# Kernel tuning notes

Hardware: AMD Instinct MI355X
Metric: run time of the kernel (lower is better)

Reference implementation:

```python
import jax, jax.numpy as jnp
import numpy as np

N = 100000
IN_DIM = 256
OUT_DIM = 256
E = 3200000
SLOPE = 0.2


def setup_inputs() -> dict:
    key = jax.random.key(0)
    ks = jax.random.split(key, 14)
    xav = lambda k, shape: jax.random.normal(k, shape, jnp.float32) * np.sqrt(2.0 / sum(shape))
    inp = {
        "H": jax.random.normal(ks[0], (N, IN_DIM), jnp.float32),
        "W0": xav(ks[1], (IN_DIM, OUT_DIM)),
        "W1": xav(ks[2], (IN_DIM, OUT_DIM)),
        "W2": xav(ks[3], (IN_DIM, OUT_DIM)),
        "a0": xav(ks[4], (2 * OUT_DIM,)),
        "a1": xav(ks[5], (2 * OUT_DIM,)),
        "a2": xav(ks[6], (2 * OUT_DIM,)),
        "bias": jnp.zeros((OUT_DIM,), jnp.float32),
    }
    for i, r in enumerate(["0", "1", "2"]):
        inp["row" + r] = jax.random.randint(ks[7 + 2 * i], (E,), 0, N, jnp.int32)
        inp["col" + r] = jax.random.randint(ks[8 + 2 * i], (E,), 0, N, jnp.int32)
    return inp


def _gat_type(H, W, a, row, col):
    # Wh: [N, out_dim]
    Wh = H @ W
    # attention logits per edge: leaky_relu(a_dst . Wh[row] + a_src . Wh[col])
    s_dst = Wh @ a[:OUT_DIM]   # [N]
    s_src = Wh @ a[OUT_DIM:]   # [N]
    e = jax.nn.leaky_relu(s_dst[row] + s_src[col], SLOPE)  # [E]
    # segment softmax over destination node (row)
    e_max = jax.ops.segment_max(e, row, num_segments=N)    # [N]
    e_shifted = jnp.exp(e - e_max[row])
    e_sum = jax.ops.segment_sum(e_shifted, row, num_segments=N)
    alpha = e_shifted / jnp.maximum(e_sum[row], 1e-12)     # [E]
    # weighted aggregation of source features into destinations
    return jax.ops.segment_sum(alpha[:, None] * Wh[col], row, num_segments=N)


def reference(H, row0, col0, row1, col1, row2, col2, W0, W1, W2, a0, a1, a2, bias):
    out = _gat_type(H, W0, a0, row0, col0)
    out = out + _gat_type(H, W1, a1, row1, col1)
    out = out + _gat_type(H, W2, a2, row2, col2)
    return out + bias
```

## Files before the change

kernel.cpp:

```cpp
#include <hip/hip_runtime.h>
#include <cstdint>
#include <cstddef>

#define DIM 256
#define SLOPE 0.2f
#define BSHIFT 8
#define SLOTS 9216
#define TILE 4096

typedef __attribute__((ext_vector_type(8))) short short8;
typedef __attribute__((ext_vector_type(4))) float f32x4;

__device__ __forceinline__ unsigned short f2bf(float f) {
  unsigned u = __float_as_uint(f);
  u += 0x7fffu + ((u >> 16) & 1u);
  return (unsigned short)(u >> 16);
}
__device__ __forceinline__ float bf2f(unsigned short h) {
  return __uint_as_float(((unsigned)h) << 16);
}

__global__ void wtrans_kernel(const float* __restrict__ W0, const float* __restrict__ W1,
                              const float* __restrict__ W2, unsigned short* __restrict__ Wt) {
  const float* W = blockIdx.y == 0 ? W0 : (blockIdx.y == 1 ? W1 : W2);
  int k = blockIdx.x, n = threadIdx.x;
  Wt[((size_t)blockIdx.y * DIM + n) * DIM + k] = f2bf(W[k * DIM + n]);
}

__global__ __launch_bounds__(256, 2) void gemm3_scores_kernel(
    const float* __restrict__ H, const unsigned short* __restrict__ Wt,
    const float* __restrict__ a0, const float* __restrict__ a1,
    const float* __restrict__ a2, unsigned short* __restrict__ Whb,
    float* __restrict__ s_dst, float* __restrict__ s_src, int N, size_t wstride) {
  __shared__ unsigned short Hs[128][264];
  __shared__ unsigned short Os[4][4][264];
  const int t = threadIdx.x;
  const int r0 = blockIdx.x * 128;
#pragma unroll
  for (int i = 0; i < 32; ++i) {
    int idx = t + i * 256;
    int row = idx >> 6;
    int c4 = idx & 63;
    int r = r0 + row;
    float4 h = (r < N) ? *(const float4*)&H[(size_t)r * DIM + c4 * 4]
                       : make_float4(0.f, 0.f, 0.f, 0.f);
    unsigned lo = (unsigned)f2bf(h.x) | ((unsigned)f2bf(h.y) << 16);
    unsigned hi = (unsigned)f2bf(h.z) | ((unsigned)f2bf(h.w) << 16);
    *(uint2*)&Hs[row][c4 * 4] = make_uint2(lo, hi);
  }
  __syncthreads();
  const int wave = t >> 6, lane = t & 63;
  const int q = lane >> 4, m = lane & 15;
  const int rowbase = wave * 32;
  short8 Af0[8], Af1[8];
#pragma unroll
  for (int k0 = 0; k0 < 8; ++k0) {
    Af0[k0] = *(const short8*)&Hs[rowbase + m][k0 * 32 + q * 8];
    Af1[k0] = *(const short8*)&Hs[rowbase + 16 + m][k0 * 32 + q * 8];
  }
  const float* aptr[3] = {a0, a1, a2};
  for (int ty = 0; ty < 3; ++ty) {
    const unsigned short* Wtt = Wt + (size_t)ty * DIM * DIM;
    const float* a = aptr[ty];
    f32x4 acc0[16], acc1[16];
#pragma unroll
    for (int j = 0; j < 16; ++j) {
      acc0[j] = (f32x4){0.f, 0.f, 0.f, 0.f};
      acc1[j] = (f32x4){0.f, 0.f, 0.f, 0.f};
    }
#pragma unroll
    for (int k0 = 0; k0 < 8; ++k0) {
#pragma unroll
      for (int j = 0; j < 16; ++j) {
        short8 Bf = *(const short8*)&Wtt[(size_t)(j * 16 + m) * DIM + k0 * 32 + q * 8];
        acc0[j] = __builtin_amdgcn_mfma_f32_16x16x32_bf16(Af0[k0], Bf, acc0[j], 0, 0, 0);
        acc1[j] = __builtin_amdgcn_mfma_f32_16x16x32_bf16(Af1[k0], Bf, acc1[j], 0, 0, 0);
      }
    }
    float pd0[4] = {0, 0, 0, 0}, ps0[4] = {0, 0, 0, 0};
    float pd1[4] = {0, 0, 0, 0}, ps1[4] = {0, 0, 0, 0};
#pragma unroll
    for (int j = 0; j < 16; ++j) {
      int col = j * 16 + m;
      float ad = a[col], as = a[DIM + col];
#pragma unroll
      for (int reg = 0; reg < 4; ++reg) {
        float v0 = acc0[j][reg], v1 = acc1[j][reg];
        pd0[reg] += v0 * ad;
        ps0[reg] += v0 * as;
        pd1[reg] += v1 * ad;
        ps1[reg] += v1 * as;
      }
    }
#pragma unroll
    for (int off = 8; off >= 1; off >>= 1) {
#pragma unroll
      for (int reg = 0; reg < 4; ++reg) {
        pd0[reg] += __shfl_down(pd0[reg], off);
        ps0[reg] += __shfl_down(ps0[reg], off);
        pd1[reg] += __shfl_down(pd1[reg], off);
        ps1[reg] += __shfl_down(ps1[reg], off);
      }
    }
    if (m == 0) {
#pragma unroll
      for (int reg = 0; reg < 4; ++reg) {
        int ra = r0 + rowbase + q * 4 + reg;
        int rb = ra + 16;
        if (ra < N) {
          s_dst[(size_t)ty * N + ra] = pd0[reg];
          s_src[(size_t)ty * N + ra] = ps0[reg];
        }
        if (rb < N) {
          s_dst[(size_t)ty * N + rb] = pd1[reg];
          s_src[(size_t)ty * N + rb] = ps1[reg];
        }
      }
    }
    unsigned short* wout = Whb + (size_t)ty * wstride;
#pragma unroll
    for (int g = 0; g < 2; ++g) {
#pragma unroll
      for (int p = 0; p < 4; ++p) {
        if (q == p) {
#pragma unroll
          for (int j = 0; j < 16; ++j)
#pragma unroll
            for (int reg = 0; reg < 4; ++reg)
              Os[wave][reg][j * 16 + m] = f2bf(g ? acc1[j][reg] : acc0[j][reg]);
        }
#pragma unroll
        for (int rr = 0; rr < 4; ++rr) {
          int r = r0 + rowbase + g * 16 + p * 4 + rr;
          if (r < N)
            *(uint2*)&wout[(size_t)r * DIM + lane * 4] =
                *(const uint2*)&Os[wave][rr][lane * 4];
        }
      }
    }
  }
}

__global__ __launch_bounds__(256, 2) void gemm_scores_kernel(
    const float* __restrict__ H, const unsigned short* __restrict__ Wt,
    const float* __restrict__ a, unsigned short* __restrict__ Whb,
    float* __restrict__ s_dst, float* __restrict__ s_src, int N) {
  __shared__ unsigned short Hs[64][264];
  __shared__ unsigned short Os[4][16][264];
  const int t = threadIdx.x;
  const int r0 = blockIdx.x * 64;
#pragma unroll
  for (int i = 0; i < 16; ++i) {
    int idx = t + i * 256;
    int row = idx >> 6;
    int c4 = idx & 63;
    int r = r0 + row;
    float4 h = (r < N) ? *(const float4*)&H[(size_t)r * DIM + c4 * 4]
                       : make_float4(0.f, 0.f, 0.f, 0.f);
    unsigned lo = (unsigned)f2bf(h.x) | ((unsigned)f2bf(h.y) << 16);
    unsigned hi = (unsigned)f2bf(h.z) | ((unsigned)f2bf(h.w) << 16);
    *(uint2*)&Hs[row][c4 * 4] = make_uint2(lo, hi);
  }
  __syncthreads();
  const int wave = t >> 6, lane = t & 63;
  const int q = lane >> 4, m = lane & 15;
  const int rowbase = wave * 16;
  short8 Af[8];
#pragma unroll
  for (int k0 = 0; k0 < 8; ++k0)
    Af[k0] = *(const short8*)&Hs[rowbase + m][k0 * 32 + q * 8];
  f32x4 acc[16];
#pragma unroll
  for (int j = 0; j < 16; ++j) acc[j] = (f32x4){0.f, 0.f, 0.f, 0.f};
#pragma unroll
  for (int k0 = 0; k0 < 8; ++k0) {
#pragma unroll
    for (int j = 0; j < 16; ++j) {
      short8 Bf = *(const short8*)&Wt[(size_t)(j * 16 + m) * DIM + k0 * 32 + q * 8];
      acc[j] = __builtin_amdgcn_mfma_f32_16x16x32_bf16(Af[k0], Bf, acc[j], 0, 0, 0);
    }
  }
  float pd[4] = {0, 0, 0, 0}, ps[4] = {0, 0, 0, 0};
#pragma unroll
  for (int j = 0; j < 16; ++j) {
    int col = j * 16 + m;
    float ad = a[col], as = a[DIM + col];
#pragma unroll
    for (int reg = 0; reg < 4; ++reg) {
      float v = acc[j][reg];
      pd[reg] += v * ad;
      ps[reg] += v * as;
      Os[wave][q * 4 + reg][col] = f2bf(v);
    }
  }
#pragma unroll
  for (int off = 8; off >= 1; off >>= 1) {
#pragma unroll
    for (int reg = 0; reg < 4; ++reg) {
      pd[reg] += __shfl_down(pd[reg], off);
      ps[reg] += __shfl_down(ps[reg], off);
    }
  }
  if (m == 0) {
#pragma unroll
    for (int reg = 0; reg < 4; ++reg) {
      int r = r0 + rowbase + q * 4 + reg;
      if (r < N) {
        s_dst[r] = pd[reg];
        s_src[r] = ps[reg];
      }
    }
  }
  __syncthreads();
#pragma unroll
  for (int row = 0; row < 16; ++row) {
    int r = r0 + rowbase + row;
    if (r < N)
      *(uint2*)&Whb[(size_t)r * DIM + lane * 4] = *(const uint2*)&Os[wave][row][lane * 4];
  }
}

__global__ __launch_bounds__(256) void bin_edges_kernel(
    const int* __restrict__ r0, const int* __restrict__ r1, const int* __restrict__ r2,
    const int* __restrict__ c0, const int* __restrict__ c1, const int* __restrict__ c2,
    int* __restrict__ bcnt,
    unsigned* __restrict__ pairs,
    int E, int NB) {
  __shared__ int hist[512];
  __shared__ int curs[512];
  const int ty = blockIdx.y;
  const int* rr = ty == 0 ? r0 : (ty == 1 ? r1 : r2);
  const int* cc = ty == 0 ? c0 : (ty == 1 ? c1 : c2);
  const int t = threadIdx.x;
  const int base = blockIdx.x * TILE;
  for (int i = t; i < NB; i += 256) hist[i] = 0;
  __syncthreads();
  int rows[TILE / 256];
#pragma unroll
  for (int i = 0; i < TILE / 256; ++i) {
    int e = base + t + i * 256;
    int r = (e < E) ? rr[e] : -1;
    rows[i] = r;
    if (r >= 0) atomicAdd(&hist[r >> BSHIFT], 1);
  }
  __syncthreads();
  for (int b = t; b < NB; b += 256) {
    int h = hist[b];
    int off = h ? atomicAdd(&bcnt[ty * NB + b], h) : 0;
    curs[b] = b * SLOTS + off;
  }
  __syncthreads();
  unsigned* pt = pairs + (size_t)ty * NB * SLOTS;
#pragma unroll
  for (int i = 0; i < TILE / 256; ++i) {
    int e = base + t + i * 256;
    if (e >= E) continue;
    int r = rows[i];
    int b = r >> BSHIFT;
    int pos = atomicAdd(&curs[b], 1);
    if (pos - b * SLOTS < SLOTS)
      pt[pos] = ((unsigned)(r & 255) << 17) | (unsigned)cc[e];
  }
}

__global__ __launch_bounds__(256) void bucket_sort_kernel(
    const int* __restrict__ bcnt, unsigned* __restrict__ pairs,
    int* __restrict__ rp, int* __restrict__ deg, int N, int NB) {
  __shared__ int hist[256];
  __shared__ int excl[256];
  __shared__ int curs[256];
  __shared__ unsigned stage[SLOTS];
  const int b = blockIdx.x, ty = blockIdx.y;
  const int t = threadIdx.x;
  int cnt = bcnt[ty * NB + b];
  if (cnt > SLOTS) cnt = SLOTS;
  unsigned* pb = pairs + (size_t)ty * NB * SLOTS + (size_t)b * SLOTS;
  hist[t] = 0;
  __syncthreads();
  for (int i = t; i < cnt; i += 256) atomicAdd(&hist[pb[i] >> 17], 1);
  __syncthreads();
  int v = hist[t];
  excl[t] = v;
  __syncthreads();
  for (int off = 1; off < 256; off <<= 1) {
    int u = (t >= off) ? excl[t - off] : 0;
    __syncthreads();
    excl[t] += u;
    __syncthreads();
  }
  int ex = excl[t] - v;
  curs[t] = ex;
  int r = (b << BSHIFT) + t;
  if (r < N) {
    rp[(size_t)ty * N + r] = b * SLOTS + ex;
    deg[(size_t)ty * N + r] = v;
  }
  __syncthreads();
  for (int i = t; i < cnt; i += 256) {
    unsigned p = pb[i];
    int pos = atomicAdd(&curs[p >> 17], 1);
    stage[pos] = p;
  }
  __syncthreads();
  for (int i = t; i < cnt; i += 256) pb[i] = stage[i];
}

__global__ __launch_bounds__(256) void gat_fused_kernel(
    const int* __restrict__ rp, const int* __restrict__ deg,
    const unsigned* __restrict__ pairs,
    const float* __restrict__ s_dst, const float* __restrict__ s_src,
    const unsigned short* __restrict__ Whb,
    const float* __restrict__ bias, float* __restrict__ out, int N, int NB,
    size_t wstride) {
  __shared__ uint2 ebuf[4][64];
  int n = (int)((blockIdx.x * (unsigned)blockDim.x + threadIdx.x) >> 6);
  if (n >= N) return;
  const int wid = (threadIdx.x >> 6);
  const int lane = threadIdx.x & 63;
  float4 total = {0.f, 0.f, 0.f, 0.f};
  for (int t = 0; t < 3; ++t) {
    int beg = rp[(size_t)t * N + n], d = deg[(size_t)t * N + n];
    if (d == 0) continue;
    int end = beg + d;
    const unsigned* pcol = pairs + (size_t)t * NB * SLOTS;
    const float* ss = s_src + (size_t)t * N;
    float sd = s_dst[(size_t)t * N + n];
    const unsigned short* wbase = Whb + (size_t)t * wstride + lane * 4;
    float mx = -__builtin_inff();
    for (int p = beg + lane; p < end; p += 64) {
      float v = sd + ss[pcol[p] & 0x1FFFFu];
      v = v > 0.f ? v : SLOPE * v;
      mx = fmaxf(mx, v);
    }
#pragma unroll
    for (int off = 32; off >= 1; off >>= 1) mx = fmaxf(mx, __shfl_down(mx, off));
    mx = __shfl(mx, 0);
    float4 acc = {0.f, 0.f, 0.f, 0.f};
    float psum = 0.f;
    for (int base = beg; base < end; base += 64) {
      int myp = base + lane;
      int cnt = end - base;
      if (cnt > 64) cnt = 64;
      unsigned myc = 0;
      float mype = 0.f;
      if (myp < end) {
        myc = pcol[myp] & 0x1FFFFu;
        float v = sd + ss[myc];
        v = v > 0.f ? v : SLOPE * v;
        mype = __expf(v - mx);
      }
      psum += mype;
      ebuf[wid][lane] = make_uint2(myc, __float_as_uint(mype));
#pragma unroll 8
      for (int j = 0; j < cnt; ++j) {
        uint2 cp = ebuf[wid][j];
        float pe = __uint_as_float(cp.y);
        ushort4 w = *(const ushort4*)&wbase[(size_t)cp.x * DIM];
        acc.x += pe * bf2f(w.x);
        acc.y += pe * bf2f(w.y);
        acc.z += pe * bf2f(w.z);
        acc.w += pe * bf2f(w.w);
      }
    }
#pragma unroll
    for (int off = 32; off >= 1; off >>= 1) psum += __shfl_down(psum, off);
    psum = __shfl(psum, 0);
    float inv = 1.f / fmaxf(psum, 1e-12f);
    total.x += acc.x * inv;
    total.y += acc.y * inv;
    total.z += acc.z * inv;
    total.w += acc.w * inv;
  }
  float4 cur = ((const float4*)bias)[lane];
  cur.x += total.x;
  cur.y += total.y;
  cur.z += total.z;
  cur.w += total.w;
  *((float4*)(out + (size_t)n * DIM) + lane) = cur;
}

__global__ __launch_bounds__(256) void gat_node_kernel(
    const int* __restrict__ rp, const int* __restrict__ deg,
    const unsigned* __restrict__ pcol,
    const float* __restrict__ s_dst, const float* __restrict__ s_src,
    const unsigned short* __restrict__ Whb,
    const float* __restrict__ bias, float* __restrict__ out, int N, int first) {
  __shared__ uint2 ebuf[4][64];
  int n = (int)((blockIdx.x * (unsigned)blockDim.x + threadIdx.x) >> 6);
  if (n >= N) return;
  const int wid = (threadIdx.x >> 6);
  const int lane = threadIdx.x & 63;
  int beg = rp[n], d = deg[n], end = beg + d;
  if (!first && d == 0) return;
  float sd = s_dst[n];
  float mx = -__builtin_inff();
  for (int p = beg + lane; p < end; p += 64) {
    float v = sd + s_src[pcol[p] & 0x1FFFFu];
    v = v > 0.f ? v : SLOPE * v;
    mx = fmaxf(mx, v);
  }
#pragma unroll
  for (int off = 32; off >= 1; off >>= 1) mx = fmaxf(mx, __shfl_down(mx, off));
  mx = __shfl(mx, 0);
  const unsigned short* wbase = Whb + lane * 4;
  float4 acc = {0.f, 0.f, 0.f, 0.f};
  float psum = 0.f;
  for (int base = beg; base < end; base += 64) {
    int myp = base + lane;
    int cnt = end - base;
    if (cnt > 64) cnt = 64;
    unsigned myc = 0;
    float mype = 0.f;
    if (myp < end) {
      myc = pcol[myp] & 0x1FFFFu;
      float v = sd + s_src[myc];
      v = v > 0.f ? v : SLOPE * v;
      mype = __expf(v - mx);
    }
    psum += mype;
    ebuf[wid][lane] = make_uint2(myc, __float_as_uint(mype));
#pragma unroll 8
    for (int j = 0; j < cnt; ++j) {
      uint2 cp = ebuf[wid][j];
      float pe = __uint_as_float(cp.y);
      ushort4 w = *(const ushort4*)&wbase[(size_t)cp.x * DIM];
      acc.x += pe * bf2f(w.x);
      acc.y += pe * bf2f(w.y);
      acc.z += pe * bf2f(w.z);
      acc.w += pe * bf2f(w.w);
    }
  }
#pragma unroll
  for (int off = 32; off >= 1; off >>= 1) psum += __shfl_down(psum, off);
  psum = __shfl(psum, 0);
  float inv = 1.f / fmaxf(psum, 1e-12f);
  float4* o = (float4*)(out + (size_t)n * DIM) + lane;
  float4 cur = first ? ((const float4*)bias)[lane] : *o;
  cur.x += acc.x * inv;
  cur.y += acc.y * inv;
  cur.z += acc.z * inv;
  cur.w += acc.w * inv;
  *o = cur;
}

static inline size_t align256(size_t x) { return (x + 255) & ~(size_t)255; }

extern "C" void kernel_launch(void* const* d_in, const int* in_sizes, int n_in,
                              void* d_out, int out_size, void* d_ws, size_t ws_size,
                              hipStream_t stream) {
  const float* H = (const float*)d_in[0];
  const float* W[3] = {(const float*)d_in[1], (const float*)d_in[2], (const float*)d_in[3]};
  const float* a[3] = {(const float*)d_in[4], (const float*)d_in[5], (const float*)d_in[6]};
  const float* bias = (const float*)d_in[7];
  const int* row[3] = {(const int*)d_in[8], (const int*)d_in[10], (const int*)d_in[12]};
  const int* col[3] = {(const int*)d_in[9], (const int*)d_in[11], (const int*)d_in[13]};
  const int N = in_sizes[0] / DIM;
  const int E = in_sizes[8];
  const int NB = (N + 255) >> BSHIFT;
  float* out = (float*)d_out;

  char* ws = (char*)d_ws;
  size_t off = 0;
  unsigned short* Wt = (unsigned short*)(ws + off);
  off = align256(off + (size_t)3 * DIM * DIM * sizeof(unsigned short));
  float* s_dst = (float*)(ws + off);
  off = align256(off + (size_t)3 * N * sizeof(float));
  float* s_src = (float*)(ws + off);
  off = align256(off + (size_t)3 * N * sizeof(float));
  int* bcnt = (int*)(ws + off);
  off = align256(off + (size_t)3 * NB * sizeof(int));
  int* rp = (int*)(ws + off);
  off = align256(off + (size_t)3 * N * sizeof(int));
  int* deg = (int*)(ws + off);
  off = align256(off + (size_t)3 * N * sizeof(int));
  unsigned* pairs = (unsigned*)(ws + off);
  off = align256(off + (size_t)3 * NB * SLOTS * sizeof(unsigned));
  unsigned short* Whb = (unsigned short*)(ws + off);
  const size_t whb_bytes = align256((size_t)N * DIM * sizeof(unsigned short));
  const size_t wstride = whb_bytes / sizeof(unsigned short);
  const int fused = (ws_size >= off + 3 * whb_bytes) ? 1 : 0;

  wtrans_kernel<<<dim3(DIM, 3), 256, 0, stream>>>(W[0], W[1], W[2], Wt);
  hipMemsetAsync(bcnt, 0, (size_t)3 * NB * sizeof(int), stream);
  const int eb = (E + TILE - 1) / TILE;
  bin_edges_kernel<<<dim3(eb, 3), 256, 0, stream>>>(row[0], row[1], row[2], col[0], col[1],
                                                    col[2], bcnt, pairs, E, NB);
  bucket_sort_kernel<<<dim3(NB, 3), 256, 0, stream>>>(bcnt, pairs, rp, deg, N, NB);

  const int gat_blocks = (N * 64 + 255) / 256;
  if (fused) {
    gemm3_scores_kernel<<<(N + 127) / 128, 256, 0, stream>>>(H, Wt, a[0], a[1], a[2], Whb,
                                                             s_dst, s_src, N, wstride);
    gat_fused_kernel<<<gat_blocks, 256, 0, stream>>>(rp, deg, pairs, s_dst, s_src, Whb, bias,
                                                     out, N, NB, wstride);
  } else {
    for (int t = 0; t < 3; ++t) {
      gemm_scores_kernel<<<(N + 63) / 64, 256, 0, stream>>>(H, Wt + (size_t)t * DIM * DIM,
                                                            a[t], Whb, s_dst + (size_t)t * N,
                                                            s_src + (size_t)t * N, N);
      gat_node_kernel<<<gat_blocks, 256, 0, stream>>>(
          rp + (size_t)t * N, deg + (size_t)t * N, pairs + (size_t)t * NB * SLOTS,
          s_dst + (size_t)t * N, s_src + (size_t)t * N, Whb, bias, out, N, t == 0 ? 1 : 0);
    }
  }
  (void)n_in;
  (void)out_size;
  (void)ws_size;
}
```

Measured before the change: 1.426 ms.

## Merge independent prep and compute stages into combined horizontal-fused kernels

Weight transpose and edge binning now run as one prep kernel, with the block index choosing the role. The GEMM with scores and the per-bucket sort likewise share one compute kernel. Independent work can then overlap on the GPU and there are fewer launches and idle tails. The cost is that the combined kernel sizes its shared memory for the larger GEMM role, about 76 KB. Sort blocks therefore get the GEMM's occupancy limits, and the mixed kernel may use more registers.

```diff
diff --git a/kernel.cpp b/kernel.cpp
--- a/kernel.cpp
+++ b/kernel.cpp
@@ -20,22 +20,94 @@
   return __uint_as_float(((unsigned)h) << 16);
 }
 
-__global__ void wtrans_kernel(const float* __restrict__ W0, const float* __restrict__ W1,
-                              const float* __restrict__ W2, unsigned short* __restrict__ Wt) {
-  const float* W = blockIdx.y == 0 ? W0 : (blockIdx.y == 1 ? W1 : W2);
-  int k = blockIdx.x, n = threadIdx.x;
-  Wt[((size_t)blockIdx.y * DIM + n) * DIM + k] = f2bf(W[k * DIM + n]);
-}
-
-__global__ __launch_bounds__(256, 2) void gemm3_scores_kernel(
-    const float* __restrict__ H, const unsigned short* __restrict__ Wt,
+
+__device__ __forceinline__ void bin_edges_body(
+    int bx, int ty, int* hist, int* curs, const int* __restrict__ rr,
+    const int* __restrict__ cc, int* __restrict__ bcnt, unsigned* __restrict__ pairs,
+    int E, int NB) {
+  const int t = threadIdx.x;
+  const int base = bx * TILE;
+  for (int i = t; i < NB; i += 256) hist[i] = 0;
+  __syncthreads();
+  int rows[TILE / 256];
+#pragma unroll
+  for (int i = 0; i < TILE / 256; ++i) {
+    int e = base + t + i * 256;
+    int r = (e < E) ? rr[e] : -1;
+    rows[i] = r;
+    if (r >= 0) atomicAdd(&hist[r >> BSHIFT], 1);
+  }
+  __syncthreads();
+  for (int b = t; b < NB; b += 256) {
+    int h = hist[b];
+    int off = h ? atomicAdd(&bcnt[ty * NB + b], h) : 0;
+    curs[b] = b * SLOTS + off;
+  }
+  __syncthreads();
+  unsigned* pt = pairs + (size_t)ty * NB * SLOTS;
+#pragma unroll
+  for (int i = 0; i < TILE / 256; ++i) {
+    int e = base + t + i * 256;
+    if (e >= E) continue;
+    int r = rows[i];
+    int b = r >> BSHIFT;
+    int pos = atomicAdd(&curs[b], 1);
+    if (pos - b * SLOTS < SLOTS)
+      pt[pos] = ((unsigned)(r & 255) << 17) | (unsigned)cc[e];
+  }
+}
+
+__device__ __forceinline__ void bsort_body(
+    int b, int ty, char* smem, const int* __restrict__ bcnt,
+    unsigned* __restrict__ pairs, int* __restrict__ rp, int* __restrict__ deg,
+    int N, int NB) {
+  int* hist = (int*)smem;
+  int* excl = hist + 256;
+  int* curs = excl + 256;
+  unsigned* stage = (unsigned*)(curs + 256);
+  const int t = threadIdx.x;
+  int cnt = bcnt[ty * NB + b];
+  if (cnt > SLOTS) cnt = SLOTS;
+  unsigned* pb = pairs + (size_t)ty * NB * SLOTS + (size_t)b * SLOTS;
+  hist[t] = 0;
+  __syncthreads();
+  for (int i = t; i < cnt; i += 256) atomicAdd(&hist[pb[i] >> 17], 1);
+  __syncthreads();
+  int v = hist[t];
+  excl[t] = v;
+  __syncthreads();
+  for (int off = 1; off < 256; off <<= 1) {
+    int u = (t >= off) ? excl[t - off] : 0;
+    __syncthreads();
+    excl[t] += u;
+    __syncthreads();
+  }
+  int ex = excl[t] - v;
+  curs[t] = ex;
+  int r = (b << BSHIFT) + t;
+  if (r < N) {
+    rp[(size_t)ty * N + r] = b * SLOTS + ex;
+    deg[(size_t)ty * N + r] = v;
+  }
+  __syncthreads();
+  for (int i = t; i < cnt; i += 256) {
+    unsigned p = pb[i];
+    int pos = atomicAdd(&curs[p >> 17], 1);
+    stage[pos] = p;
+  }
+  __syncthreads();
+  for (int i = t; i < cnt; i += 256) pb[i] = stage[i];
+}
+
+__device__ __forceinline__ void gemm3_body(
+    int bx, char* smem, const float* __restrict__ H, const unsigned short* __restrict__ Wt,
     const float* __restrict__ a0, const float* __restrict__ a1,
     const float* __restrict__ a2, unsigned short* __restrict__ Whb,
     float* __restrict__ s_dst, float* __restrict__ s_src, int N, size_t wstride) {
-  __shared__ unsigned short Hs[128][264];
-  __shared__ unsigned short Os[4][4][264];
+  unsigned short(*Hs)[264] = (unsigned short(*)[264])smem;
+  unsigned short(*Os)[4][264] = (unsigned short(*)[4][264])(smem + 128 * 264 * 2);
   const int t = threadIdx.x;
-  const int r0 = blockIdx.x * 128;
+  const int r0 = bx * 128;
 #pragma unroll
   for (int i = 0; i < 32; ++i) {
     int idx = t + i * 256;
@@ -141,6 +213,52 @@
   }
 }
 
+
+__global__ __launch_bounds__(256) void prep_kernel(
+    const float* __restrict__ W0, const float* __restrict__ W1,
+    const float* __restrict__ W2, unsigned short* __restrict__ Wt,
+    const int* __restrict__ r0, const int* __restrict__ r1, const int* __restrict__ r2,
+    const int* __restrict__ c0, const int* __restrict__ c1, const int* __restrict__ c2,
+    int* __restrict__ bcnt, unsigned* __restrict__ pairs, int E, int NB, int eb) {
+  __shared__ int smem[1024];
+  const int bx = blockIdx.x;
+  if (bx < 768) {
+    int ty = bx >> 8, k = bx & 255, n = threadIdx.x;
+    const float* W = ty == 0 ? W0 : (ty == 1 ? W1 : W2);
+    Wt[((size_t)ty * DIM + n) * DIM + k] = f2bf(W[k * DIM + n]);
+    return;
+  }
+  int e2 = bx - 768;
+  int ty = e2 / eb, bxx = e2 % eb;
+  const int* rr = ty == 0 ? r0 : (ty == 1 ? r1 : r2);
+  const int* cc = ty == 0 ? c0 : (ty == 1 ? c1 : c2);
+  bin_edges_body(bxx, ty, smem, smem + 512, rr, cc, bcnt, pairs, E, NB);
+}
+
+__global__ __launch_bounds__(256, 2) void compute_kernel(
+    const float* __restrict__ H, const unsigned short* __restrict__ Wt,
+    const float* __restrict__ a0, const float* __restrict__ a1,
+    const float* __restrict__ a2, unsigned short* __restrict__ Whb,
+    float* __restrict__ s_dst, float* __restrict__ s_src, int N, size_t wstride,
+    const int* __restrict__ bcnt, unsigned* __restrict__ pairs,
+    int* __restrict__ rp, int* __restrict__ deg, int NB, int gemm_blocks) {
+  __shared__ __align__(16) char smem[76032];
+  const int bx = blockIdx.x;
+  if (bx < gemm_blocks) {
+    gemm3_body(bx, smem, H, Wt, a0, a1, a2, Whb, s_dst, s_src, N, wstride);
+  } else {
+    int e = bx - gemm_blocks;
+    bsort_body(e % NB, e / NB, smem, bcnt, pairs, rp, deg, N, NB);
+  }
+}
+
+__global__ __launch_bounds__(256) void bucket_sort_kernel(
+    const int* __restrict__ bcnt, unsigned* __restrict__ pairs,
+    int* __restrict__ rp, int* __restrict__ deg, int N, int NB) {
+  __shared__ __align__(16) char smem[39936];
+  bsort_body(blockIdx.x, blockIdx.y, smem, bcnt, pairs, rp, deg, N, NB);
+}
+
 __global__ __launch_bounds__(256, 2) void gemm_scores_kernel(
     const float* __restrict__ H, const unsigned short* __restrict__ Wt,
     const float* __restrict__ a, unsigned short* __restrict__ Whb,
@@ -218,91 +336,6 @@
     if (r < N)
       *(uint2*)&Whb[(size_t)r * DIM + lane * 4] = *(const uint2*)&Os[wave][row][lane * 4];
   }
-}
-
-__global__ __launch_bounds__(256) void bin_edges_kernel(
-    const int* __restrict__ r0, const int* __restrict__ r1, const int* __restrict__ r2,
-    const int* __restrict__ c0, const int* __restrict__ c1, const int* __restrict__ c2,
-    int* __restrict__ bcnt,
-    unsigned* __restrict__ pairs,
-    int E, int NB) {
-  __shared__ int hist[512];
-  __shared__ int curs[512];
-  const int ty = blockIdx.y;
-  const int* rr = ty == 0 ? r0 : (ty == 1 ? r1 : r2);
-  const int* cc = ty == 0 ? c0 : (ty == 1 ? c1 : c2);
-  const int t = threadIdx.x;
-  const int base = blockIdx.x * TILE;
-  for (int i = t; i < NB; i += 256) hist[i] = 0;
-  __syncthreads();
-  int rows[TILE / 256];
-#pragma unroll
-  for (int i = 0; i < TILE / 256; ++i) {
-    int e = base + t + i * 256;
-    int r = (e < E) ? rr[e] : -1;
-    rows[i] = r;
-    if (r >= 0) atomicAdd(&hist[r >> BSHIFT], 1);
-  }
-  __syncthreads();
-  for (int b = t; b < NB; b += 256) {
-    int h = hist[b];
-    int off = h ? atomicAdd(&bcnt[ty * NB + b], h) : 0;
-    curs[b] = b * SLOTS + off;
-  }
-  __syncthreads();
-  unsigned* pt = pairs + (size_t)ty * NB * SLOTS;
-#pragma unroll
-  for (int i = 0; i < TILE / 256; ++i) {
-    int e = base + t + i * 256;
-    if (e >= E) continue;
-    int r = rows[i];
-    int b = r >> BSHIFT;
-    int pos = atomicAdd(&curs[b], 1);
-    if (pos - b * SLOTS < SLOTS)
-      pt[pos] = ((unsigned)(r & 255) << 17) | (unsigned)cc[e];
-  }
-}
-
-__global__ __launch_bounds__(256) void bucket_sort_kernel(
-    const int* __restrict__ bcnt, unsigned* __restrict__ pairs,
-    int* __restrict__ rp, int* __restrict__ deg, int N, int NB) {
-  __shared__ int hist[256];
-  __shared__ int excl[256];
-  __shared__ int curs[256];
-  __shared__ unsigned stage[SLOTS];
-  const int b = blockIdx.x, ty = blockIdx.y;
-  const int t = threadIdx.x;
-  int cnt = bcnt[ty * NB + b];
-  if (cnt > SLOTS) cnt = SLOTS;
-  unsigned* pb = pairs + (size_t)ty * NB * SLOTS + (size_t)b * SLOTS;
-  hist[t] = 0;
-  __syncthreads();
-  for (int i = t; i < cnt; i += 256) atomicAdd(&hist[pb[i] >> 17], 1);
-  __syncthreads();
-  int v = hist[t];
-  excl[t] = v;
-  __syncthreads();
-  for (int off = 1; off < 256; off <<= 1) {
-    int u = (t >= off) ? excl[t - off] : 0;
-    __syncthreads();
-    excl[t] += u;
-    __syncthreads();
-  }
-  int ex = excl[t] - v;
-  curs[t] = ex;
-  int r = (b << BSHIFT) + t;
-  if (r < N) {
-    rp[(size_t)ty * N + r] = b * SLOTS + ex;
-    deg[(size_t)ty * N + r] = v;
-  }
-  __syncthreads();
-  for (int i = t; i < cnt; i += 256) {
-    unsigned p = pb[i];
-    int pos = atomicAdd(&curs[p >> 17], 1);
-    stage[pos] = p;
-  }
-  __syncthreads();
-  for (int i = t; i < cnt; i += 256) pb[i] = stage[i];
 }
 
 __global__ __launch_bounds__(256) void gat_fused_kernel(
@@ -480,20 +513,21 @@
   const size_t wstride = whb_bytes / sizeof(unsigned short);
   const int fused = (ws_size >= off + 3 * whb_bytes) ? 1 : 0;
 
-  wtrans_kernel<<<dim3(DIM, 3), 256, 0, stream>>>(W[0], W[1], W[2], Wt);
+  const int eb = (E + TILE - 1) / TILE;
   hipMemsetAsync(bcnt, 0, (size_t)3 * NB * sizeof(int), stream);
-  const int eb = (E + TILE - 1) / TILE;
-  bin_edges_kernel<<<dim3(eb, 3), 256, 0, stream>>>(row[0], row[1], row[2], col[0], col[1],
-                                                    col[2], bcnt, pairs, E, NB);
-  bucket_sort_kernel<<<dim3(NB, 3), 256, 0, stream>>>(bcnt, pairs, rp, deg, N, NB);
+  prep_kernel<<<768 + 3 * eb, 256, 0, stream>>>(W[0], W[1], W[2], Wt, row[0], row[1], row[2],
+                                                col[0], col[1], col[2], bcnt, pairs, E, NB, eb);
 
   const int gat_blocks = (N * 64 + 255) / 256;
   if (fused) {
-    gemm3_scores_kernel<<<(N + 127) / 128, 256, 0, stream>>>(H, Wt, a[0], a[1], a[2], Whb,
-                                                             s_dst, s_src, N, wstride);
+    const int gemm_blocks = (N + 127) / 128;
+    compute_kernel<<<gemm_blocks + 3 * NB, 256, 0, stream>>>(
+        H, Wt, a[0], a[1], a[2], Whb, s_dst, s_src, N, wstride, bcnt, pairs, rp, deg, NB,
+        gemm_blocks);
     gat_fused_kernel<<<gat_blocks, 256, 0, stream>>>(rp, deg, pairs, s_dst, s_src, Whb, bias,
                                                      out, N, NB, wstride);
   } else {
+    bucket_sort_kernel<<<dim3(NB, 3), 256, 0, stream>>>(bcnt, pairs, rp, deg, N, NB);
     for (int t = 0; t < 3; ++t) {
       gemm_scores_kernel<<<(N + 63) / 64, 256, 0, stream>>>(H, Wt + (size_t)t * DIM * DIM,
                                                             a[t], Whb, s_dst + (size_t)t * N,
```

Result: faster. 1.387 ms (-2.7%).
